# Kernel tuning notes

Measured on AMD Instinct MI355X. Metric: run time of the kernel, lower is better.

Reference implementation:

```python
import jax, jax.numpy as jnp
import numpy as np

D = 32          # max_delay_block
NEG_INF = -1e13 # matches module's self.neg_inf


def setup_inputs() -> dict:
    key = jax.random.key(0)
    ks = jax.random.split(key, 8)
    b, c, t, f, h = 2, 128, 512, 64, 32
    xm = jax.random.normal(ks[0], (b, c, t, f), dtype=jnp.float32)
    xf = jax.random.normal(ks[1], (b, c, t, f), dtype=jnp.float32)
    # pointwise_conv1 / pointwise_conv2: 1x1 convs == per-pixel linear maps c->h
    w1 = jax.random.normal(ks[2], (c, h), dtype=jnp.float32) * (1.0 / np.sqrt(c))
    b1 = jax.random.normal(ks[3], (h,), dtype=jnp.float32) * 0.01
    w2 = jax.random.normal(ks[4], (c, h), dtype=jnp.float32) * (1.0 / np.sqrt(c))
    b2 = jax.random.normal(ks[5], (h,), dtype=jnp.float32) * 0.01
    # conv2d: h -> 1 channels, kernel (5,3)   (OIHW layout)
    wc = jax.random.normal(ks[6], (1, h, 5, 3), dtype=jnp.float32) * (1.0 / np.sqrt(h * 15))
    bc = jax.random.normal(ks[7], (1,), dtype=jnp.float32) * 0.01
    return {"xm": xm, "xf": xf, "w1": w1, "b1": b1, "w2": w2, "b2": b2, "wc": wc, "bc": bc}


def reference(xm, xf, w1, b1, w2, b2, wc, bc):
    b, c, t, f = xf.shape
    # 1x1 convs (per time-freq bin linear projections)
    xm1 = jnp.einsum('bctf,ch->bhtf', xm, w1) + b1[None, :, None, None]
    xf1 = jnp.einsum('bctf,ch->bhtf', xf, w2) + b2[None, :, None, None]

    # delay windows: window j at frame i looks at original frame i + j - (D-1)
    # (j = D-1 is zero delay, j = 0 is delay D-1; out-of-range frames are zero-padded)
    idx = jnp.arange(t)[:, None] + jnp.arange(D)[None, :]          # [t, D] into padded time
    xf1p = jnp.pad(xf1, ((0, 0), (0, 0), (D - 1, 0), (0, 0)))      # [b,h,t+D-1,f]
    win = xf1p[:, :, idx, :]                                       # [b,h,t,D,f]
    corr = jnp.einsum('bhtf,bhtdf->bhtd', xm1, win)                # [b,h,t,D]

    # conv2d smoothing: kernel (5,3), pad (3,1) -> height t+2, keep first t rows
    corr1 = jax.lax.conv_general_dilated(
        corr, wc, window_strides=(1, 1), padding=((3, 3), (1, 1)),
        dimension_numbers=('NCHW', 'OIHW', 'NCHW'))
    corr1 = corr1[:, 0, :t, :] + bc[0]                             # [b,t,D]

    # causal mask: frame i cannot attend to delays pointing before frame 0,
    # i.e. positions with i + j < D - 1 get neg_inf (exactly tril().flip() logic)
    bad = (jnp.arange(t)[:, None] + jnp.arange(D)[None, :]) < (D - 1)
    corr1 = jnp.where(bad[None, :, :], NEG_INF, corr1)
    w = jax.nn.softmax(corr1, axis=-1)                             # [b,t,D]

    # delay-weighted sum over the raw far-end features
    xfp = jnp.pad(xf, ((0, 0), (0, 0), (D - 1, 0), (0, 0)))        # [b,c,t+D-1,f]
    win2 = xfp[:, :, idx, :]                                       # [b,c,t,D,f]
    out = jnp.einsum('btd,bctdf->bctf', w, win2)                   # [b,c,t,f]
    return out
```

## Files before the change

kernel.cpp:

```cpp
#include <hip/hip_runtime.h>

typedef unsigned short u16;
typedef unsigned int   u32;

#define B_ 2
#define C_ 128
#define T_ 512
#define F_ 64
#define H_ 32
#define D_ 32

#define XM1_OUT 0u
#define XF1_OUT 2097152u

#define CORR_OFF 0u
#define WQ_OFF   1127168u

__global__ __launch_bounds__(256) void k1_proj(const float* __restrict__ xm, const float* __restrict__ xf,
                                               const float* __restrict__ w1, const float* __restrict__ b1,
                                               const float* __restrict__ w2, const float* __restrict__ b2,
                                               float* __restrict__ xm1, float* __restrict__ xf1){
  int blk  = blockIdx.x;
  int mblk = blk & 127;
  int bt   = blk >> 7;
  int b    = bt >> 1, sel = bt & 1;
  int m    = mblk * 256 + threadIdx.x;

  const float* X    = (sel ? xf : xm) + (size_t)b * (C_*T_*F_) + m;
  const float* W    = sel ? w2 : w1;
  const float* bias = sel ? b2 : b1;

  float acc[H_];
#pragma unroll
  for (int h = 0; h < H_; h++) acc[h] = 0.f;

  for (int c0 = 0; c0 < C_; c0 += 16){
    float xv[16];
#pragma unroll
    for (int u = 0; u < 16; u++)
      xv[u] = X[(size_t)(c0 + u) * (T_*F_)];
#pragma unroll
    for (int u = 0; u < 16; u++){
      const float* Wr = W + (c0 + u) * H_;
#pragma unroll
      for (int h = 0; h < H_; h++) acc[h] = fmaf(xv[u], Wr[h], acc[h]);
    }
  }

  float* O = (sel ? xf1 : xm1) + (size_t)b * (H_*T_*F_) + m;
#pragma unroll
  for (int h = 0; h < H_; h++) O[(size_t)h * (T_*F_)] = acc[h] + bias[h];
}

__global__ __launch_bounds__(256) void k2_corr(const float* __restrict__ xm1, const float* __restrict__ xf1,
                                               float* __restrict__ corr_pad){
  int blk = blockIdx.x;
  int tt = blk & 7, h = (blk >> 3) & 31, b = blk >> 8;
  int t0 = tt * 64;
  const float* A  = xm1 + ((size_t)(b*H_ + h)) * (T_*F_);
  const float* Bm = xf1 + ((size_t)(b*H_ + h)) * (T_*F_);

  __shared__ float Al[64*68];
  __shared__ float Bl[95*68];
  int tid = threadIdx.x;

  for (int idx = tid; idx < 64*16; idx += 256){
    int r = idx >> 4, q = idx & 15;
    *(float4*)(Al + r*68 + q*4) = *(const float4*)(A + (size_t)(t0 + r)*F_ + q*4);
  }
  for (int idx = tid; idx < 95*16; idx += 256){
    int r = idx >> 4, q = idx & 15;
    int gr = t0 - 31 + r;
    float4 v = make_float4(0.f,0.f,0.f,0.f);
    if (gr >= 0) v = *(const float4*)(Bm + (size_t)gr*F_ + q*4);
    *(float4*)(Bl + r*68 + q*4) = v;
  }
  __syncthreads();

  int tl = tid >> 2, dg = tid & 3;
  float acc[8];
#pragma unroll
  for (int j = 0; j < 8; j++) acc[j] = 0.f;

  for (int fq = 0; fq < 16; fq++){
    float4 a = *(const float4*)(Al + tl*68 + fq*4);
#pragma unroll
    for (int j = 0; j < 8; j++){
      float4 bv = *(const float4*)(Bl + (tl + dg*8 + j)*68 + fq*4);
      acc[j] += a.x*bv.x + a.y*bv.y + a.z*bv.z + a.w*bv.w;
    }
  }
  float* o = corr_pad + ((size_t)(b*H_ + h))*(518*34) + (size_t)(t0 + tl + 3)*34 + (dg*8 + 1);
#pragma unroll
  for (int j = 0; j < 8; j++) o[j] = acc[j];
}

__global__ __launch_bounds__(256) void k3_conv_softmax(const float* __restrict__ corr_pad,
                                                       const float* __restrict__ wc, const float* __restrict__ bc,
                                                       float* __restrict__ wq){
  int b  = blockIdx.x >> 6;
  int t0 = (blockIdx.x & 63) * 8;
  int tid = threadIdx.x;

  __shared__ float ls[32*12*34];
  const float* cp = corr_pad + (size_t)b * (H_*518*34);
  for (int idx = tid; idx < 32*12*34; idx += 256){
    int h = idx / 408, rem = idx - h*408;
    int r = rem / 34, dd = rem - r*34;
    int gr = t0 + r;
    bool halo = (gr < 3) | (gr > 514) | (dd == 0) | (dd == 33);
    ls[idx] = halo ? 0.f : cp[(size_t)h*(518*34) + (size_t)gr*34 + dd];
  }
  __syncthreads();

  int tl = tid >> 5, d = tid & 31;
  int t = t0 + tl;

  float val = bc[0];
  for (int h = 0; h < H_; h++){
    const float* base = ls + h*408 + tl*34 + d;
    const float* wch = wc + h*15;
#pragma unroll
    for (int kh = 0; kh < 5; kh++){
#pragma unroll
      for (int kw = 0; kw < 3; kw++){
        val += base[kh*34 + kw] * wch[kh*3 + kw];
      }
    }
  }
  if (t + d < D_ - 1) val = -1e13f;

  float m = val;
#pragma unroll
  for (int off = 16; off > 0; off >>= 1) m = fmaxf(m, __shfl_xor(m, off));
  float e = __expf(val - m);
  float s = e;
#pragma unroll
  for (int off = 16; off > 0; off >>= 1) s += __shfl_xor(s, off);

  wq[((size_t)b*T_ + t)*D_ + d] = e / s;
}

__global__ __launch_bounds__(256) void k4_out(const float* __restrict__ xf, const float* __restrict__ wq,
                                              float* __restrict__ out){
  int blk = blockIdx.x;
  int tt = blk & 7, c = (blk >> 3) & 127, b = blk >> 10;
  int t0 = tt * 64;
  const float* Xf = xf + ((size_t)(b*C_ + c)) * (T_*F_);

  __shared__ float xfl[95*68];
  __shared__ float wl[64*33];
  int tid = threadIdx.x;

  for (int idx = tid; idx < 95*16; idx += 256){
    int r = idx >> 4, q = idx & 15;
    int gr = t0 - 31 + r;
    float4 v = make_float4(0.f,0.f,0.f,0.f);
    if (gr >= 0) v = *(const float4*)(Xf + (size_t)gr*F_ + q*4);
    *(float4*)(xfl + r*68 + q*4) = v;
  }
  for (int idx = tid; idx < 64*8; idx += 256){
    int r = idx >> 3, q = idx & 7;
    float4 v = *(const float4*)(wq + ((size_t)b*T_ + t0 + r)*D_ + q*4);
    wl[r*33 + q*4 + 0] = v.x; wl[r*33 + q*4 + 1] = v.y;
    wl[r*33 + q*4 + 2] = v.z; wl[r*33 + q*4 + 3] = v.w;
  }
  __syncthreads();

  int tg = tid >> 4, q = tid & 15;
  float4 acc[4];
#pragma unroll
  for (int j = 0; j < 4; j++) acc[j] = make_float4(0.f,0.f,0.f,0.f);

#pragma unroll
  for (int rr = 0; rr < 35; rr++){
    float4 xv = *(const float4*)(xfl + (tg*4 + rr)*68 + q*4);
#pragma unroll
    for (int j = 0; j < 4; j++){
      int d = rr - j;
      if (d >= 0 && d < D_){
        float wv = wl[(tg*4 + j)*33 + d];
        acc[j].x += wv * xv.x; acc[j].y += wv * xv.y;
        acc[j].z += wv * xv.z; acc[j].w += wv * xv.w;
      }
    }
  }
#pragma unroll
  for (int j = 0; j < 4; j++){
    int t = t0 + tg*4 + j;
    float* O = out + (((size_t)(b*C_ + c))*T_ + t)*F_ + q*4;
    *(float4*)O = acc[j];
  }
}

extern "C" void kernel_launch(void* const* d_in, const int* in_sizes, int n_in,
                              void* d_out, int out_size, void* d_ws, size_t ws_size,
                              hipStream_t stream) {
  const float* xm = (const float*)d_in[0];
  const float* xf = (const float*)d_in[1];
  const float* w1 = (const float*)d_in[2];
  const float* b1 = (const float*)d_in[3];
  const float* w2 = (const float*)d_in[4];
  const float* b2 = (const float*)d_in[5];
  const float* wc = (const float*)d_in[6];
  const float* bc = (const float*)d_in[7];
  float* ws = (float*)d_ws;

  float* xm1 = (float*)d_out + XM1_OUT;
  float* xf1 = (float*)d_out + XF1_OUT;

  hipLaunchKernelGGL(k1_proj, dim3(512), dim3(256), 0, stream, xm, xf, w1, b1, w2, b2, xm1, xf1);
  hipLaunchKernelGGL(k2_corr, dim3(512), dim3(256), 0, stream, xm1, xf1, ws + CORR_OFF);
  hipLaunchKernelGGL(k3_conv_softmax, dim3(128), dim3(256), 0, stream, ws + CORR_OFF, wc, bc, ws + WQ_OFF);
  hipLaunchKernelGGL(k4_out, dim3(2048), dim3(256), 0, stream, xf, ws + WQ_OFF, (float*)d_out);
}
```

Baseline: 184.0 us.

## Double-buffer projection inputs into LDS via async global-to-LDS loads

```diff
diff --git a/kernel.cpp b/kernel.cpp
--- a/kernel.cpp
+++ b/kernel.cpp
@@ -15,6 +15,11 @@
 
 #define CORR_OFF 0u
 #define WQ_OFF   1127168u
+
+__device__ __forceinline__ void gl_lds16(const float* g, float* l){
+  __builtin_amdgcn_global_load_lds((const __attribute__((address_space(1))) void*)g,
+                                   (__attribute__((address_space(3))) void*)l, 16, 0, 0);
+}
 
 __global__ __launch_bounds__(256) void k1_proj(const float* __restrict__ xm, const float* __restrict__ xf,
                                                const float* __restrict__ w1, const float* __restrict__ b1,
@@ -24,32 +29,51 @@
   int mblk = blk & 127;
   int bt   = blk >> 7;
   int b    = bt >> 1, sel = bt & 1;
-  int m    = mblk * 256 + threadIdx.x;
-
-  const float* X    = (sel ? xf : xm) + (size_t)b * (C_*T_*F_) + m;
+  int m0   = mblk * 256;
+  int tid  = threadIdx.x;
+  int wave = tid >> 6, lane = tid & 63;
+
+  const float* X    = (sel ? xf : xm) + (size_t)b * (C_*T_*F_) + m0;
   const float* W    = sel ? w2 : w1;
   const float* bias = sel ? b2 : b1;
 
+  __shared__ float ls[2][32*256];
+
+#define K1_STAGE(buf, c0) do {                                            \
+    _Pragma("unroll")                                                     \
+    for (int i_ = 0; i_ < 8; i_++){                                       \
+      int r_ = (wave << 3) + i_;                                          \
+      gl_lds16(X + (size_t)((c0) + r_) * (T_*F_) + (lane << 2),           \
+               &ls[buf][r_ * 256]);                                       \
+    }                                                                     \
+  } while (0)
+
   float acc[H_];
 #pragma unroll
   for (int h = 0; h < H_; h++) acc[h] = 0.f;
 
-  for (int c0 = 0; c0 < C_; c0 += 16){
-    float xv[16];
-#pragma unroll
-    for (int u = 0; u < 16; u++)
-      xv[u] = X[(size_t)(c0 + u) * (T_*F_)];
-#pragma unroll
-    for (int u = 0; u < 16; u++){
-      const float* Wr = W + (c0 + u) * H_;
-#pragma unroll
-      for (int h = 0; h < H_; h++) acc[h] = fmaf(xv[u], Wr[h], acc[h]);
-    }
-  }
-
-  float* O = (sel ? xf1 : xm1) + (size_t)b * (H_*T_*F_) + m;
+  K1_STAGE(0, 0);
+  __syncthreads();
+
+  int cur = 0;
+  for (int k = 0; k < 4; k++){
+    if (k < 3) K1_STAGE(cur ^ 1, 32*(k+1));
+    int c0 = 32*k;
+#pragma unroll 4
+    for (int u = 0; u < 32; u++){
+      float x = ls[cur][u*256 + tid];
+      const float* Wr = W + (size_t)(c0 + u) * H_;
+#pragma unroll
+      for (int h = 0; h < H_; h++) acc[h] = fmaf(x, Wr[h], acc[h]);
+    }
+    __syncthreads();
+    cur ^= 1;
+  }
+
+  float* O = (sel ? xf1 : xm1) + (size_t)b * (H_*T_*F_) + m0 + tid;
 #pragma unroll
   for (int h = 0; h < H_; h++) O[(size_t)h * (T_*F_)] = acc[h] + bias[h];
+#undef K1_STAGE
 }
 
 __global__ __launch_bounds__(256) void k2_corr(const float* __restrict__ xm1, const float* __restrict__ xf1,
```

Measured after the change: 181.7 us. Within noise of the previous version (-1.3%).
